# Kernel optimization log

Hardware: AMD Instinct MI355X
Metric: run time of the kernel (lower is better)

The kernel has to match this reference:

```python
import math
import jax, jax.numpy as jnp
import numpy as np

B, L, D, H, DK = 2, 2048, 1024, 16, 64
LATTICE = (4, 4)


def _build_neighbours(n_heads, shape):
    positions = [divmod(i, shape[1]) for i in range(n_heads)]
    idx = np.full((n_heads, 8), -1, dtype=np.int32)
    w = np.zeros((n_heads, 8), dtype=np.float32)
    for i, (r1, c1) in enumerate(positions):
        k = 0
        for dr in (-1, 0, 1):
            for dc in (-1, 0, 1):
                if dr == 0 and dc == 0:
                    continue
                if k >= 8:
                    break
                tgt = (r1 + dr, c1 + dc)
                for j, p in enumerate(positions):
                    if p == tgt:
                        idx[i, k] = j
                        w[i, k] = math.exp(-math.hypot(dr, dc))
                        k += 1
                        break
    return idx, w


def setup_inputs() -> dict:
    key = jax.random.key(0)
    ks = jax.random.split(key, 8)
    s = 1.0 / math.sqrt(D)  # typical linear init scale
    nb_idx, nb_w = _build_neighbours(H, LATTICE)
    return {
        "query": jax.random.normal(ks[0], (B, L, D), jnp.float32),
        "key": jax.random.normal(ks[1], (B, L, D), jnp.float32),
        "value": jax.random.normal(ks[2], (B, L, D), jnp.float32),
        "Wq": jax.random.normal(ks[3], (H, DK, D), jnp.float32) * s,
        "Wk": jax.random.normal(ks[4], (H, DK, D), jnp.float32) * s,
        "Wv": jax.random.normal(ks[5], (H, DK, D), jnp.float32) * s,
        "coupling_strength": jnp.full((H,), 0.1, jnp.float32),
        "out_w": jax.random.normal(ks[6], (D, D), jnp.float32) * s,
        "out_b": jnp.zeros((D,), jnp.float32),
        "neighbour_w": jnp.asarray(nb_w),
        "mask": jax.random.randint(ks[7], (B, L), 0, 2, jnp.int32),
        "neighbour_idx": jnp.asarray(nb_idx),
    }


def _phases(coupling_strength, neighbour_idx, neighbour_w):
    # Sequential Kuramoto update over heads (order matters: earlier heads'
    # updated phases are visible to later heads, as in the torch loop).
    freq = 1.0 + 0.1 * jnp.arange(H, dtype=jnp.float32)
    ph = jnp.zeros((H,), jnp.float32)
    two_pi = 2.0 * math.pi
    for i in range(H):  # H=16, structurally distinct sequential states
        nb = jnp.clip(neighbour_idx[i], 0, H - 1)  # invalid slots have w==0
        coupling = jnp.sum(neighbour_w[i] * jnp.sin(ph[nb] - ph[i]))
        new = jnp.mod(ph[i] + 0.01 * (freq[i] + coupling_strength[i] * coupling), two_pi)
        ph = ph.at[i].set(new)
    return ph


def reference(query, key, value, Wq, Wk, Wv, coupling_strength, out_w, out_b,
              neighbour_w, mask, neighbour_idx):
    ph = _phases(coupling_strength, neighbour_idx, neighbour_w)
    bias = 0.1 * jnp.cos(ph)  # [H] per-head scalar bias

    # Batched per-head projections: [B,L,D] x [H,DK,D] -> [B,H,L,DK]
    Q = jnp.einsum('bld,hkd->bhlk', query, Wq)
    K = jnp.einsum('bld,hkd->bhlk', key, Wk)
    V = jnp.einsum('bld,hkd->bhlk', value, Wv)

    scale = math.sqrt(float(DK))
    scores = jnp.einsum('bhqd,bhkd->bhqk', Q, K) / scale  # [B,H,L,L]
    scores = scores + bias[None, :, None, None]
    m = mask[:, None, None, :]  # [B,1,1,L], matches mask.unsqueeze(1).unsqueeze(1)
    scores = jnp.where(m == 0, jnp.float32(-10000.0), scores)
    attn = jax.nn.softmax(scores, axis=-1)
    out = jnp.einsum('bhqk,bhkd->bhqd', attn, V)  # [B,H,L,DK]
    out = out.transpose(0, 2, 1, 3).reshape(B, L, H * DK)  # concat heads
    return out @ out_w.T + out_b
```

## Files before the change

kernel.cpp:

```cpp
#include <hip/hip_runtime.h>
#include <hip/hip_fp16.h>


#define B_ 2
#define L_ 2048
#define D_ 1024
#define H_ 16
#define DK_ 64

#define QSCALE 0.1803368801111244f
#define MASKOFF -14427.0f

typedef _Float16 f16;
typedef _Float16 f16x2 __attribute__((ext_vector_type(2)));
typedef _Float16 f16x4 __attribute__((ext_vector_type(4)));
typedef _Float16 f16x8 __attribute__((ext_vector_type(8)));
typedef __fp16 hf16x2 __attribute__((ext_vector_type(2)));
typedef float f32x4 __attribute__((ext_vector_type(4)));

__global__ __launch_bounds__(256) void qkv_proj_kernel(
    const float* __restrict__ query, const float* __restrict__ keyx,
    const float* __restrict__ value,
    const float* __restrict__ Wq, const float* __restrict__ Wk,
    const float* __restrict__ Wv,
    f16* __restrict__ Qh, f16* __restrict__ Kh, f16* __restrict__ VhT)
{
    const int z = blockIdx.z;
    const float* X = (z == 0) ? query : (z == 1) ? keyx : value;
    const float* W = (z == 0) ? Wq : (z == 1) ? Wk : Wv;
    f16* out = (z == 0) ? Qh : (z == 1) ? Kh : VhT;
    const float qs = (z == 0) ? QSCALE : 1.0f;

    const int m0 = blockIdx.x * 128;
    const int n0 = blockIdx.y * 128;
    const int tid = threadIdx.x;
    const int lane = tid & 63;
    const int w = tid >> 6;
    const int wr = (w >> 1) * 64, wc = (w & 1) * 64;

    __shared__ f16 As[128 * 40];
    __shared__ f16 Ws[128 * 40];

    f32x4 acc[4][4] = {};

    for (int kk = 0; kk < D_; kk += 32) {
        __syncthreads();
        {
            int r = tid >> 3;
            int c = (tid & 7) * 4;
            #pragma unroll
            for (int p = 0; p < 4; ++p) {
                int row = p * 32 + r;
                float4 va = *(const float4*)&X[(size_t)(m0 + row) * D_ + kk + c];
                f16x4 ha = { (f16)(va.x * qs), (f16)(va.y * qs), (f16)(va.z * qs), (f16)(va.w * qs) };
                *(f16x4*)&As[row * 40 + c] = ha;
                float4 vb = *(const float4*)&W[(size_t)(n0 + row) * D_ + kk + c];
                f16x4 hb = { (f16)vb.x, (f16)vb.y, (f16)vb.z, (f16)vb.w };
                *(f16x4*)&Ws[row * 40 + c] = hb;
            }
        }
        __syncthreads();

        f16x8 af[4], bf[4];
        const int lg = (lane >> 4) * 8;
        #pragma unroll
        for (int i = 0; i < 4; ++i) {
            af[i] = *(const f16x8*)&As[(wr + i * 16 + (lane & 15)) * 40 + lg];
            bf[i] = *(const f16x8*)&Ws[(wc + i * 16 + (lane & 15)) * 40 + lg];
        }
        #pragma unroll
        for (int i = 0; i < 4; ++i)
            #pragma unroll
            for (int j = 0; j < 4; ++j)
                acc[i][j] = __builtin_amdgcn_mfma_f32_16x16x32_f16(af[i], bf[j], acc[i][j], 0, 0, 0);
    }

    if (z == 2) {
        #pragma unroll
        for (int i = 0; i < 4; ++i) {
            int grow = m0 + wr + i * 16 + (lane >> 4) * 4;
            int b = grow >> 11, l = grow & (L_ - 1);
            #pragma unroll
            for (int j = 0; j < 4; ++j) {
                int gcol = n0 + wc + j * 16 + (lane & 15);
                int hh = gcol >> 6, k = gcol & 63;
                f16x4 o = { (f16)acc[i][j][0], (f16)acc[i][j][1],
                            (f16)acc[i][j][2], (f16)acc[i][j][3] };
                *(f16x4*)&out[((size_t)((b * H_ + hh) * DK_ + k)) * L_ + l] = o;
            }
        }
    } else {
        #pragma unroll
        for (int i = 0; i < 4; ++i) {
            int grow = m0 + wr + i * 16 + (lane >> 4) * 4;
            #pragma unroll
            for (int j = 0; j < 4; ++j) {
                int gcol = n0 + wc + j * 16 + (lane & 15);
                int hh = gcol >> 6, k = gcol & 63;
                #pragma unroll
                for (int r = 0; r < 4; ++r) {
                    int row = grow + r;
                    int b = row >> 11, l = row & (L_ - 1);
                    out[(((size_t)(b * H_ + hh)) * L_ + l) * DK_ + k] = (f16)acc[i][j][r];
                }
            }
        }
    }
}

__global__ __launch_bounds__(256) void attn_kernel(
    const f16* __restrict__ Qh, const f16* __restrict__ Kh,
    const f16* __restrict__ VhT, const int* __restrict__ mask,
    f16* __restrict__ Oh)
{
    const int n = blockIdx.x;
    const int bh = ((n >> 7) << 3) + (n & 7);
    const int qb = (n >> 3) & 15;
    const int b = bh >> 4, h = bh & 15;
    const int q0 = qb * 128;
    const int tid = threadIdx.x;
    const int lane = tid & 63;
    const int w = tid >> 6;
    const int lq = lane & 15, g = lane >> 4;

    __shared__ f16 Ks[64 * 72];
    __shared__ f16 Vt[64 * 72];
    __shared__ f16 Plds[4][32 * 72];
    __shared__ float mofft[64];

    const size_t base = (size_t)bh * L_ * DK_;
    const int* maskp = mask + b * L_;

    f16x8 qf0[2], qf1[2];
    {
        const f16* qptr = Qh + base + (size_t)(q0 + w * 32 + lq) * DK_ + g * 8;
        qf0[0] = *(const f16x8*)(qptr);
        qf0[1] = *(const f16x8*)(qptr + 32);
        qptr += 16 * DK_;
        qf1[0] = *(const f16x8*)(qptr);
        qf1[1] = *(const f16x8*)(qptr + 32);
    }

    const int srow = tid >> 2, scol = (tid & 3) * 16;

    f32x4 acc0[4] = {}, acc1[4] = {};
    float mrun0 = -1e30f, lrun0 = 0.f;
    float mrun1 = -1e30f, lrun1 = 0.f;

    f16x8 kA0, kA1, vA0, vA1;
    f16x8 kB0, kB1, vB0, vB1;

    auto issue = [&](int k0, f16x8& k0r, f16x8& k1r, f16x8& v0r, f16x8& v1r) {
        const f16* kp = Kh + base + (size_t)(k0 + srow) * DK_ + scol;
        k0r = *(const f16x8*)kp;
        k1r = *(const f16x8*)(kp + 8);
        const f16* vp = VhT + (size_t)(bh * DK_ + srow) * L_ + k0 + scol;
        v0r = *(const f16x8*)vp;
        v1r = *(const f16x8*)(vp + 8);
    };

    auto store_tile = [&](int k0, const f16x8& k0r, const f16x8& k1r,
                          const f16x8& v0r, const f16x8& v1r) {
        *(f16x8*)&Ks[srow * 72 + scol] = k0r;
        *(f16x8*)&Ks[srow * 72 + scol + 8] = k1r;
        *(f16x8*)&Vt[srow * 72 + scol] = v0r;
        *(f16x8*)&Vt[srow * 72 + scol + 8] = v1r;
        if (tid < 16) {
            int4 mv = *(const int4*)&maskp[k0 + tid * 4];
            float4 f = { mv.x ? 0.f : MASKOFF, mv.y ? 0.f : MASKOFF,
                         mv.z ? 0.f : MASKOFF, mv.w ? 0.f : MASKOFF };
            *(float4*)&mofft[tid * 4] = f;
        }
    };

    auto softmax_store = [&](float* sv, float& mrun, float& lrun,
                             f32x4* acc, int rowoff) {
        float a0 = fmaxf(sv[0], sv[1]),  a1 = fmaxf(sv[2], sv[3]);
        float a2 = fmaxf(sv[4], sv[5]),  a3 = fmaxf(sv[6], sv[7]);
        float a4 = fmaxf(sv[8], sv[9]),  a5 = fmaxf(sv[10], sv[11]);
        float a6 = fmaxf(sv[12], sv[13]), a7 = fmaxf(sv[14], sv[15]);
        float m = fmaxf(fmaxf(fmaxf(a0, a1), fmaxf(a2, a3)),
                        fmaxf(fmaxf(a4, a5), fmaxf(a6, a7)));
        m = fmaxf(m, __shfl_xor(m, 16, 64));
        m = fmaxf(m, __shfl_xor(m, 32, 64));
        if (__any(m > mrun)) {
            float mn = fmaxf(mrun, m);
            float scl = exp2f(mrun - mn);
            mrun = mn;
            lrun *= scl;
            #pragma unroll
            for (int f = 0; f < 4; ++f) acc[f] *= scl;
        }
        f16* pl = (f16*)Plds[w];
        float ls0 = 0.f, ls1 = 0.f;
        #pragma unroll
        for (int kt = 0; kt < 4; ++kt) {
            float p0 = exp2f(sv[kt * 4 + 0] - mrun);
            float p1 = exp2f(sv[kt * 4 + 1] - mrun);
            float p2 = exp2f(sv[kt * 4 + 2] - mrun);
            float p3 = exp2f(sv[kt * 4 + 3] - mrun);
            ls0 += p0 + p1;
            ls1 += p2 + p3;
            hf16x2 lo = __builtin_amdgcn_cvt_pkrtz(p0, p1);
            hf16x2 hi = __builtin_amdgcn_cvt_pkrtz(p2, p3);
            f16x2 lo2 = __builtin_bit_cast(f16x2, lo);
            f16x2 hi2 = __builtin_bit_cast(f16x2, hi);
            f16x4 pk; pk[0] = lo2[0]; pk[1] = lo2[1]; pk[2] = hi2[0]; pk[3] = hi2[1];
            *(f16x4*)&pl[(rowoff + lq) * 72 + kt * 16 + g * 4] = pk;
        }
        float ls = ls0 + ls1;
        ls += __shfl_xor(ls, 16, 64);
        ls += __shfl_xor(ls, 32, 64);
        lrun += ls;
    };

    auto compute = [&]() {
        float sv0[16], sv1[16];
        __builtin_amdgcn_s_setprio(1);
        #pragma unroll
        for (int kt = 0; kt < 4; ++kt) {
            f32x4 c = *(const f32x4*)&mofft[kt * 16 + g * 4];
            const f16* ka = &Ks[(kt * 16 + lq) * 72 + g * 8];
            f16x8 a0 = *(const f16x8*)ka;
            f16x8 a1 = *(const f16x8*)(ka + 32);
            f32x4 s0 = __builtin_amdgcn_mfma_f32_16x16x32_f16(a0, qf0[0], c, 0, 0, 0);
            s0 = __builtin_amdgcn_mfma_f32_16x16x32_f16(a1, qf0[1], s0, 0, 0, 0);
            f32x4 s1 = __builtin_amdgcn_mfma_f32_16x16x32_f16(a0, qf1[0], c, 0, 0, 0);
            s1 = __builtin_amdgcn_mfma_f32_16x16x32_f16(a1, qf1[1], s1, 0, 0, 0);
            *(f32x4*)&sv0[kt * 4] = s0;
            *(f32x4*)&sv1[kt * 4] = s1;
        }
        __builtin_amdgcn_s_setprio(0);

        softmax_store(sv0, mrun0, lrun0, acc0, 0);
        softmax_store(sv1, mrun1, lrun1, acc1, 16);
        asm volatile("s_waitcnt lgkmcnt(0)" ::: "memory");
        __builtin_amdgcn_sched_barrier(0);

        f16* pl = (f16*)Plds[w];
        __builtin_amdgcn_s_setprio(1);
        #pragma unroll
        for (int kc = 0; kc < 2; ++kc) {
            f16x8 pb0 = *(const f16x8*)&pl[lq * 72 + kc * 32 + g * 8];
            f16x8 pb1 = *(const f16x8*)&pl[(16 + lq) * 72 + kc * 32 + g * 8];
            #pragma unroll
            for (int f = 0; f < 4; ++f) {
                f16x8 va = *(const f16x8*)&Vt[(f * 16 + lq) * 72 + kc * 32 + g * 8];
                acc0[f] = __builtin_amdgcn_mfma_f32_16x16x32_f16(va, pb0, acc0[f], 0, 0, 0);
                acc1[f] = __builtin_amdgcn_mfma_f32_16x16x32_f16(va, pb1, acc1[f], 0, 0, 0);
            }
        }
        __builtin_amdgcn_s_setprio(0);
    };

    issue(0, kA0, kA1, vA0, vA1);
    for (int k0 = 0; k0 < L_; k0 += 128) {
        __syncthreads();
        store_tile(k0, kA0, kA1, vA0, vA1);
        issue(k0 + 64, kB0, kB1, vB0, vB1);
        __syncthreads();
        compute();

        __syncthreads();
        store_tile(k0 + 64, kB0, kB1, vB0, vB1);
        if (k0 + 128 < L_) issue(k0 + 128, kA0, kA1, vA0, vA1);
        __syncthreads();
        compute();
    }

    {
        float inv = 1.f / lrun0;
        int q = q0 + w * 32 + lq;
        #pragma unroll
        for (int f = 0; f < 4; ++f) {
            f16x4 o = { (f16)(acc0[f][0] * inv), (f16)(acc0[f][1] * inv),
                        (f16)(acc0[f][2] * inv), (f16)(acc0[f][3] * inv) };
            *(f16x4*)&Oh[((size_t)(b * L_ + q)) * D_ + h * 64 + f * 16 + g * 4] = o;
        }
    }
    {
        float inv = 1.f / lrun1;
        int q = q0 + w * 32 + 16 + lq;
        #pragma unroll
        for (int f = 0; f < 4; ++f) {
            f16x4 o = { (f16)(acc1[f][0] * inv), (f16)(acc1[f][1] * inv),
                        (f16)(acc1[f][2] * inv), (f16)(acc1[f][3] * inv) };
            *(f16x4*)&Oh[((size_t)(b * L_ + q)) * D_ + h * 64 + f * 16 + g * 4] = o;
        }
    }
}

__global__ __launch_bounds__(256) void out_proj_kernel(
    const f16* __restrict__ Oh, const float* __restrict__ outw,
    const float* __restrict__ outb, float* __restrict__ Y)
{
    const int m0 = blockIdx.x * 128;
    const int n0 = blockIdx.y * 128;
    const int tid = threadIdx.x;
    const int lane = tid & 63;
    const int w = tid >> 6;
    const int wr = (w >> 1) * 64, wc = (w & 1) * 64;

    __shared__ f16 As[128 * 40];
    __shared__ f16 Ws[128 * 40];

    f32x4 acc[4][4] = {};

    for (int kk = 0; kk < D_; kk += 32) {
        __syncthreads();
        {
            int r = tid >> 3;
            int c = (tid & 7) * 4;
            #pragma unroll
            for (int p = 0; p < 4; ++p) {
                int row = p * 32 + r;
                f16x4 ha = *(const f16x4*)&Oh[(size_t)(m0 + row) * D_ + kk + c];
                *(f16x4*)&As[row * 40 + c] = ha;
                float4 vb = *(const float4*)&outw[(size_t)(n0 + row) * D_ + kk + c];
                f16x4 hb = { (f16)vb.x, (f16)vb.y, (f16)vb.z, (f16)vb.w };
                *(f16x4*)&Ws[row * 40 + c] = hb;
            }
        }
        __syncthreads();

        f16x8 af[4], bf[4];
        const int lg = (lane >> 4) * 8;
        #pragma unroll
        for (int i = 0; i < 4; ++i) {
            af[i] = *(const f16x8*)&As[(wr + i * 16 + (lane & 15)) * 40 + lg];
            bf[i] = *(const f16x8*)&Ws[(wc + i * 16 + (lane & 15)) * 40 + lg];
        }
        #pragma unroll
        for (int i = 0; i < 4; ++i)
            #pragma unroll
            for (int j = 0; j < 4; ++j)
                acc[i][j] = __builtin_amdgcn_mfma_f32_16x16x32_f16(af[i], bf[j], acc[i][j], 0, 0, 0);
    }

    #pragma unroll
    for (int i = 0; i < 4; ++i) {
        int grow = m0 + wr + i * 16 + (lane >> 4) * 4;
        #pragma unroll
        for (int j = 0; j < 4; ++j) {
            int gcol = n0 + wc + j * 16 + (lane & 15);
            float bias = outb[gcol];
            #pragma unroll
            for (int r = 0; r < 4; ++r)
                Y[(size_t)(grow + r) * D_ + gcol] = acc[i][j][r] + bias;
        }
    }
}

extern "C" void kernel_launch(void* const* d_in, const int* in_sizes, int n_in,
                              void* d_out, int out_size, void* d_ws, size_t ws_size,
                              hipStream_t stream) {
    const float* query = (const float*)d_in[0];
    const float* key   = (const float*)d_in[1];
    const float* value = (const float*)d_in[2];
    const float* Wq    = (const float*)d_in[3];
    const float* Wk    = (const float*)d_in[4];
    const float* Wv    = (const float*)d_in[5];
    const float* outw  = (const float*)d_in[7];
    const float* outb  = (const float*)d_in[8];
    const int*   mask  = (const int*)d_in[10];
    float* Y = (float*)d_out;

    char* ws = (char*)d_ws;
    f16* Qh  = (f16*)(ws);
    f16* Kh  = (f16*)(ws + 8388608);
    f16* VhT = (f16*)(ws + 16777216);
    f16* Oh  = (f16*)(ws + 25165824);

    qkv_proj_kernel<<<dim3(32, 8, 3), 256, 0, stream>>>(query, key, value,
                                                        Wq, Wk, Wv, Qh, Kh, VhT);
    attn_kernel<<<dim3(512), 256, 0, stream>>>(Qh, Kh, VhT, mask, Oh);
    out_proj_kernel<<<dim3(32, 8), 256, 0, stream>>>(Oh, outw, outb, Y);
}
```

Baseline: 179.9 us.

## Load K/V fragments directly from global in attention; prefetch GEMM tiles into registers

The attention kernel drops its shared-memory K/V staging and block-wide barriers. Each wave now reads its K and V MFMA fragments straight from global memory (relying on L2 for reuse across waves) and precomputes the full mask offset row per wave in LDS. The block-to-(batch,head) mapping is also changed to keep each head's blocks on one XCD. Both projection GEMMs gain register prefetch of the next k-slice, so global loads overlap the MFMA work. This trades LDS reuse for more global/L2 traffic and uses a larger LDS allocation for the mask.

```diff
diff --git a/kernel.cpp b/kernel.cpp
--- a/kernel.cpp
+++ b/kernel.cpp
@@ -43,22 +43,33 @@
 
     f32x4 acc[4][4] = {};
 
+    const int r = tid >> 3, c = (tid & 7) * 4;
+    float4 ra[4], rb[4];
+
+    auto issueK = [&](int kk) {
+        #pragma unroll
+        for (int p = 0; p < 4; ++p) {
+            ra[p] = *(const float4*)&X[(size_t)(m0 + p * 32 + r) * D_ + kk + c];
+            rb[p] = *(const float4*)&W[(size_t)(n0 + p * 32 + r) * D_ + kk + c];
+        }
+    };
+    auto storeK = [&]() {
+        #pragma unroll
+        for (int p = 0; p < 4; ++p) {
+            int row = p * 32 + r;
+            f16x4 ha = { (f16)(ra[p].x * qs), (f16)(ra[p].y * qs),
+                         (f16)(ra[p].z * qs), (f16)(ra[p].w * qs) };
+            *(f16x4*)&As[row * 40 + c] = ha;
+            f16x4 hb = { (f16)rb[p].x, (f16)rb[p].y, (f16)rb[p].z, (f16)rb[p].w };
+            *(f16x4*)&Ws[row * 40 + c] = hb;
+        }
+    };
+
+    issueK(0);
     for (int kk = 0; kk < D_; kk += 32) {
         __syncthreads();
-        {
-            int r = tid >> 3;
-            int c = (tid & 7) * 4;
-            #pragma unroll
-            for (int p = 0; p < 4; ++p) {
-                int row = p * 32 + r;
-                float4 va = *(const float4*)&X[(size_t)(m0 + row) * D_ + kk + c];
-                f16x4 ha = { (f16)(va.x * qs), (f16)(va.y * qs), (f16)(va.z * qs), (f16)(va.w * qs) };
-                *(f16x4*)&As[row * 40 + c] = ha;
-                float4 vb = *(const float4*)&W[(size_t)(n0 + row) * D_ + kk + c];
-                f16x4 hb = { (f16)vb.x, (f16)vb.y, (f16)vb.z, (f16)vb.w };
-                *(f16x4*)&Ws[row * 40 + c] = hb;
-            }
-        }
+        storeK();
+        if (kk + 32 < D_) issueK(kk + 32);
         __syncthreads();
 
         f16x8 af[4], bf[4];
@@ -98,10 +109,10 @@
                 int gcol = n0 + wc + j * 16 + (lane & 15);
                 int hh = gcol >> 6, k = gcol & 63;
                 #pragma unroll
-                for (int r = 0; r < 4; ++r) {
-                    int row = grow + r;
+                for (int rr = 0; rr < 4; ++rr) {
+                    int row = grow + rr;
                     int b = row >> 11, l = row & (L_ - 1);
-                    out[(((size_t)(b * H_ + hh)) * L_ + l) * DK_ + k] = (f16)acc[i][j][r];
+                    out[(((size_t)(b * H_ + hh)) * L_ + l) * DK_ + k] = (f16)acc[i][j][rr];
                 }
             }
         }
@@ -114,26 +125,35 @@
     f16* __restrict__ Oh)
 {
     const int n = blockIdx.x;
-    const int bh = ((n >> 7) << 3) + (n & 7);
-    const int qb = (n >> 3) & 15;
+    const int xcd = n & 7, idx = n >> 3;
+    const int bh  = xcd * 4 + (idx >> 4);
+    const int qblk = idx & 15;
     const int b = bh >> 4, h = bh & 15;
-    const int q0 = qb * 128;
-    const int tid = threadIdx.x;
-    const int lane = tid & 63;
-    const int w = tid >> 6;
+    const int tid = threadIdx.x, lane = tid & 63, w = tid >> 6;
+    const int q0 = qblk * 128 + w * 32;
     const int lq = lane & 15, g = lane >> 4;
 
-    __shared__ f16 Ks[64 * 72];
-    __shared__ f16 Vt[64 * 72];
     __shared__ f16 Plds[4][32 * 72];
-    __shared__ float mofft[64];
-
-    const size_t base = (size_t)bh * L_ * DK_;
+    __shared__ float Moff[4][L_];
+
+    f16* pl = (f16*)Plds[w];
+    float* mo = (float*)Moff[w];
+
+    const size_t base = (size_t)bh * (L_ * DK_);
     const int* maskp = mask + b * L_;
+
+    #pragma unroll
+    for (int ch = 0; ch < 8; ++ch) {
+        int i = ch * 256 + lane * 4;
+        int4 mv = *(const int4*)&maskp[i];
+        float4 f = { mv.x ? 0.f : MASKOFF, mv.y ? 0.f : MASKOFF,
+                     mv.z ? 0.f : MASKOFF, mv.w ? 0.f : MASKOFF };
+        *(float4*)&mo[i] = f;
+    }
 
     f16x8 qf0[2], qf1[2];
     {
-        const f16* qptr = Qh + base + (size_t)(q0 + w * 32 + lq) * DK_ + g * 8;
+        const f16* qptr = Qh + base + (size_t)(q0 + lq) * DK_ + g * 8;
         qf0[0] = *(const f16x8*)(qptr);
         qf0[1] = *(const f16x8*)(qptr + 32);
         qptr += 16 * DK_;
@@ -141,37 +161,9 @@
         qf1[1] = *(const f16x8*)(qptr + 32);
     }
 
-    const int srow = tid >> 2, scol = (tid & 3) * 16;
-
     f32x4 acc0[4] = {}, acc1[4] = {};
     float mrun0 = -1e30f, lrun0 = 0.f;
     float mrun1 = -1e30f, lrun1 = 0.f;
-
-    f16x8 kA0, kA1, vA0, vA1;
-    f16x8 kB0, kB1, vB0, vB1;
-
-    auto issue = [&](int k0, f16x8& k0r, f16x8& k1r, f16x8& v0r, f16x8& v1r) {
-        const f16* kp = Kh + base + (size_t)(k0 + srow) * DK_ + scol;
-        k0r = *(const f16x8*)kp;
-        k1r = *(const f16x8*)(kp + 8);
-        const f16* vp = VhT + (size_t)(bh * DK_ + srow) * L_ + k0 + scol;
-        v0r = *(const f16x8*)vp;
-        v1r = *(const f16x8*)(vp + 8);
-    };
-
-    auto store_tile = [&](int k0, const f16x8& k0r, const f16x8& k1r,
-                          const f16x8& v0r, const f16x8& v1r) {
-        *(f16x8*)&Ks[srow * 72 + scol] = k0r;
-        *(f16x8*)&Ks[srow * 72 + scol + 8] = k1r;
-        *(f16x8*)&Vt[srow * 72 + scol] = v0r;
-        *(f16x8*)&Vt[srow * 72 + scol + 8] = v1r;
-        if (tid < 16) {
-            int4 mv = *(const int4*)&maskp[k0 + tid * 4];
-            float4 f = { mv.x ? 0.f : MASKOFF, mv.y ? 0.f : MASKOFF,
-                         mv.z ? 0.f : MASKOFF, mv.w ? 0.f : MASKOFF };
-            *(float4*)&mofft[tid * 4] = f;
-        }
-    };
 
     auto softmax_store = [&](float* sv, float& mrun, float& lrun,
                              f32x4* acc, int rowoff) {
@@ -191,7 +183,6 @@
             #pragma unroll
             for (int f = 0; f < 4; ++f) acc[f] *= scl;
         }
-        f16* pl = (f16*)Plds[w];
         float ls0 = 0.f, ls1 = 0.f;
         #pragma unroll
         for (int kt = 0; kt < 4; ++kt) {
@@ -214,30 +205,42 @@
         lrun += ls;
     };
 
-    auto compute = [&]() {
+    #pragma unroll 2
+    for (int k0 = 0; k0 < L_; k0 += 64) {
+        f16x8 vfr[4][2];
+        {
+            const f16* vp = VhT + (size_t)(bh * DK_ + lq) * L_ + k0 + g * 8;
+            #pragma unroll
+            for (int f = 0; f < 4; ++f) {
+                vfr[f][0] = *(const f16x8*)(vp + (size_t)f * 16 * L_);
+                vfr[f][1] = *(const f16x8*)(vp + (size_t)f * 16 * L_ + 32);
+            }
+        }
+
         float sv0[16], sv1[16];
-        __builtin_amdgcn_s_setprio(1);
-        #pragma unroll
-        for (int kt = 0; kt < 4; ++kt) {
-            f32x4 c = *(const f32x4*)&mofft[kt * 16 + g * 4];
-            const f16* ka = &Ks[(kt * 16 + lq) * 72 + g * 8];
-            f16x8 a0 = *(const f16x8*)ka;
-            f16x8 a1 = *(const f16x8*)(ka + 32);
-            f32x4 s0 = __builtin_amdgcn_mfma_f32_16x16x32_f16(a0, qf0[0], c, 0, 0, 0);
-            s0 = __builtin_amdgcn_mfma_f32_16x16x32_f16(a1, qf0[1], s0, 0, 0, 0);
-            f32x4 s1 = __builtin_amdgcn_mfma_f32_16x16x32_f16(a0, qf1[0], c, 0, 0, 0);
-            s1 = __builtin_amdgcn_mfma_f32_16x16x32_f16(a1, qf1[1], s1, 0, 0, 0);
-            *(f32x4*)&sv0[kt * 4] = s0;
-            *(f32x4*)&sv1[kt * 4] = s1;
-        }
-        __builtin_amdgcn_s_setprio(0);
+        {
+            const f16* kp = Kh + base + (size_t)(k0 + lq) * DK_ + g * 8;
+            __builtin_amdgcn_s_setprio(1);
+            #pragma unroll
+            for (int kt = 0; kt < 4; ++kt) {
+                f16x8 a0 = *(const f16x8*)(kp + kt * 16 * DK_);
+                f16x8 a1 = *(const f16x8*)(kp + kt * 16 * DK_ + 32);
+                f32x4 cin = *(const f32x4*)&mo[k0 + kt * 16 + g * 4];
+                f32x4 s0 = __builtin_amdgcn_mfma_f32_16x16x32_f16(a0, qf0[0], cin, 0, 0, 0);
+                s0 = __builtin_amdgcn_mfma_f32_16x16x32_f16(a1, qf0[1], s0, 0, 0, 0);
+                f32x4 s1 = __builtin_amdgcn_mfma_f32_16x16x32_f16(a0, qf1[0], cin, 0, 0, 0);
+                s1 = __builtin_amdgcn_mfma_f32_16x16x32_f16(a1, qf1[1], s1, 0, 0, 0);
+                *(f32x4*)&sv0[kt * 4] = s0;
+                *(f32x4*)&sv1[kt * 4] = s1;
+            }
+            __builtin_amdgcn_s_setprio(0);
+        }
 
         softmax_store(sv0, mrun0, lrun0, acc0, 0);
         softmax_store(sv1, mrun1, lrun1, acc1, 16);
         asm volatile("s_waitcnt lgkmcnt(0)" ::: "memory");
         __builtin_amdgcn_sched_barrier(0);
 
-        f16* pl = (f16*)Plds[w];
         __builtin_amdgcn_s_setprio(1);
         #pragma unroll
         for (int kc = 0; kc < 2; ++kc) {
@@ -245,32 +248,16 @@
             f16x8 pb1 = *(const f16x8*)&pl[(16 + lq) * 72 + kc * 32 + g * 8];
             #pragma unroll
             for (int f = 0; f < 4; ++f) {
-                f16x8 va = *(const f16x8*)&Vt[(f * 16 + lq) * 72 + kc * 32 + g * 8];
-                acc0[f] = __builtin_amdgcn_mfma_f32_16x16x32_f16(va, pb0, acc0[f], 0, 0, 0);
-                acc1[f] = __builtin_amdgcn_mfma_f32_16x16x32_f16(va, pb1, acc1[f], 0, 0, 0);
+                acc0[f] = __builtin_amdgcn_mfma_f32_16x16x32_f16(vfr[f][kc], pb0, acc0[f], 0, 0, 0);
+                acc1[f] = __builtin_amdgcn_mfma_f32_16x16x32_f16(vfr[f][kc], pb1, acc1[f], 0, 0, 0);
             }
         }
         __builtin_amdgcn_s_setprio(0);
-    };
-
-    issue(0, kA0, kA1, vA0, vA1);
-    for (int k0 = 0; k0 < L_; k0 += 128) {
-        __syncthreads();
-        store_tile(k0, kA0, kA1, vA0, vA1);
-        issue(k0 + 64, kB0, kB1, vB0, vB1);
-        __syncthreads();
-        compute();
-
-        __syncthreads();
-        store_tile(k0 + 64, kB0, kB1, vB0, vB1);
-        if (k0 + 128 < L_) issue(k0 + 128, kA0, kA1, vA0, vA1);
-        __syncthreads();
-        compute();
     }
 
     {
         float inv = 1.f / lrun0;
-        int q = q0 + w * 32 + lq;
+        int q = q0 + lq;
         #pragma unroll
         for (int f = 0; f < 4; ++f) {
             f16x4 o = { (f16)(acc0[f][0] * inv), (f16)(acc0[f][1] * inv),
@@ -280,7 +267,7 @@
     }
     {
         float inv = 1.f / lrun1;
-        int q = q0 + w * 32 + 16 + lq;
+        int q = q0 + 16 + lq;
         #pragma unroll
         for (int f = 0; f < 4; ++f) {
             f16x4 o = { (f16)(acc1[f][0] * inv), (f16)(acc1[f][1] * inv),
@@ -306,21 +293,32 @@
 
     f32x4 acc[4][4] = {};
 
+    const int r = tid >> 3, c = (tid & 7) * 4;
+    f16x4 ra[4];
+    float4 rb[4];
+
+    auto issueK = [&](int kk) {
+        #pragma unroll
+        for (int p = 0; p < 4; ++p) {
+            ra[p] = *(const f16x4*)&Oh[(size_t)(m0 + p * 32 + r) * D_ + kk + c];
+            rb[p] = *(const float4*)&outw[(size_t)(n0 + p * 32 + r) * D_ + kk + c];
+        }
+    };
+    auto storeK = [&]() {
+        #pragma unroll
+        for (int p = 0; p < 4; ++p) {
+            int row = p * 32 + r;
+            *(f16x4*)&As[row * 40 + c] = ra[p];
+            f16x4 hb = { (f16)rb[p].x, (f16)rb[p].y, (f16)rb[p].z, (f16)rb[p].w };
+            *(f16x4*)&Ws[row * 40 + c] = hb;
+        }
+    };
+
+    issueK(0);
     for (int kk = 0; kk < D_; kk += 32) {
         __syncthreads();
-        {
-            int r = tid >> 3;
-            int c = (tid & 7) * 4;
-            #pragma unroll
-            for (int p = 0; p < 4; ++p) {
-                int row = p * 32 + r;
-                f16x4 ha = *(const f16x4*)&Oh[(size_t)(m0 + row) * D_ + kk + c];
-                *(f16x4*)&As[row * 40 + c] = ha;
-                float4 vb = *(const float4*)&outw[(size_t)(n0 + row) * D_ + kk + c];
-                f16x4 hb = { (f16)vb.x, (f16)vb.y, (f16)vb.z, (f16)vb.w };
-                *(f16x4*)&Ws[row * 40 + c] = hb;
-            }
-        }
+        storeK();
+        if (kk + 32 < D_) issueK(kk + 32);
         __syncthreads();
 
         f16x8 af[4], bf[4];
@@ -345,8 +343,8 @@
             int gcol = n0 + wc + j * 16 + (lane & 15);
             float bias = outb[gcol];
             #pragma unroll
-            for (int r = 0; r < 4; ++r)
-                Y[(size_t)(grow + r) * D_ + gcol] = acc[i][j][r] + bias;
+            for (int rr = 0; rr < 4; ++rr)
+                Y[(size_t)(grow + rr) * D_ + gcol] = acc[i][j][rr] + bias;
         }
     }
 }
```

New measurement: 210.9 us. +17.2%, slower.
